# Kernel optimization log

Measured on AMD Instinct MI355X. Metric: run time of the kernel, lower is better.

## Reference

```python
import jax, jax.numpy as jnp
import numpy as np

EMB = 1024
HEADS = 16
HEAD_DIM = EMB // HEADS
BLOCK = 256
N_GLOBAL = 4
WINDOW = 128
ROPE_BASE = 10000.0


def rotate_half(x):
    # interleaved rotate: (-x2_0, x1_0, -x2_1, x1_1, ...), faithful to source
    x1 = x[..., ::2]
    x2 = x[..., 1::2]
    return jnp.stack((-x2, x1), axis=-1).reshape(x.shape)


def setup_inputs() -> dict:
    key = jax.random.key(0)
    k0, k1, k2 = jax.random.split(key, 3)
    B, S = 2, 2048
    x = jax.random.normal(k0, (B, S, EMB), dtype=jnp.float32)
    # Linear weights stored as [in, out]; y = x @ W (bias=False in source)
    w_qkv = jax.random.normal(k1, (EMB, 3 * EMB), dtype=jnp.float32) * (EMB ** -0.5)
    w_out = jax.random.normal(k2, (EMB, EMB), dtype=jnp.float32) * (EMB ** -0.5)
    return {"x": x, "w_qkv": w_qkv, "w_out": w_out}


def _forward(x, w_qkv, w_out):
    B, S, E = x.shape
    H, D = HEADS, HEAD_DIM
    qkv = (x @ w_qkv).reshape(B, S, 3, H, D).transpose(2, 0, 3, 1, 4)  # [3,B,H,S,D]
    q, k, v = qkv[0], qkv[1], qkv[2]

    # Rotary embedding (start_pos = 0, no cache)
    inv_freq = 1.0 / (ROPE_BASE ** (jnp.arange(0, D, 2, dtype=jnp.float32) / D))
    pos = jnp.arange(S, dtype=jnp.float32)
    freqs = jnp.outer(pos, inv_freq)                 # [S, D/2]
    emb = jnp.concatenate([freqs, freqs], axis=-1)   # [S, D]
    cos = jnp.cos(emb)[None, None]                   # [1,1,S,D]
    sin = jnp.sin(emb)[None, None]
    q = q * cos + rotate_half(q) * sin
    k = k * cos + rotate_half(k) * sin

    # Block-local + global-token + sliding-window mask, AND causal (vectorized)
    i = jnp.arange(S)[:, None]
    j = jnp.arange(S)[None, :]
    allowed = (i // BLOCK == j // BLOCK) | (i < N_GLOBAL) | (j < N_GLOBAL) \
              | (jnp.abs(i - j) <= WINDOW)
    allowed = allowed & (j <= i)
    # NOTE: source passes ~mask to F.scaled_dot_product_attention, where a
    # boolean attn_mask with True means "attend". We replicate that exactly.
    attend = ~allowed  # [S, S]

    scale = D ** -0.5
    scores = jnp.einsum("bhsd,bhtd->bhst", q, k) * scale      # [B,H,S,S]
    scores = jnp.where(attend[None, None], scores, jnp.float32(-1e30))
    attn = jax.nn.softmax(scores, axis=-1)
    out = jnp.einsum("bhst,bhtd->bhsd", attn, v)              # [B,H,S,D]
    out = out.transpose(0, 2, 1, 3).reshape(B, S, E)
    return out @ w_out


def reference(x, w_qkv, w_out):
    return _forward(x, w_qkv, w_out)
```

## Files before the change

kernel.cpp:

```cpp
#include <hip/hip_runtime.h>
#include <hip/hip_bf16.h>

#define EMBD   1024
#define NHEAD  16
#define HDIM   64
#define SEQ    2048
#define BATCH  2
#define MROWS  4096
#define NQKV   3072
#define VSTR   2064

using floatx4 = __attribute__((ext_vector_type(4))) float;
using short8  = __attribute__((ext_vector_type(8))) short;

static __device__ __forceinline__ float bf2f(unsigned short u) {
    unsigned int v = ((unsigned int)u) << 16;
    return __uint_as_float(v);
}
static __device__ __forceinline__ unsigned short f2bf(float f) {
    __hip_bfloat16 h = __float2bfloat16(f);
    return *reinterpret_cast<unsigned short*>(&h);
}

__global__ __launch_bounds__(256) void cast_x(
    const float* __restrict__ x, unsigned short* __restrict__ xh,
    unsigned short* __restrict__ xl)
{
    int idx = (blockIdx.x * 256 + threadIdx.x) * 4;
    float4 v = *(const float4*)(x + idx);
    ushort4 h, l;
    h.x = f2bf(v.x); l.x = f2bf(v.x - bf2f(h.x));
    h.y = f2bf(v.y); l.y = f2bf(v.y - bf2f(h.y));
    h.z = f2bf(v.z); l.z = f2bf(v.z - bf2f(h.z));
    h.w = f2bf(v.w); l.w = f2bf(v.w - bf2f(h.w));
    *(ushort4*)(xh + idx) = h;
    *(ushort4*)(xl + idx) = l;
}

__global__ __launch_bounds__(256) void cast_wT(
    const float* __restrict__ w, unsigned short* __restrict__ wT, int N)
{
    __shared__ unsigned short th[64][65];
    const int k0 = blockIdx.y * 64, n0 = blockIdx.x * 64;
    const int t = threadIdx.x;
    const int r = t >> 4, c = (t & 15) * 4;
    for (int rr = r; rr < 64; rr += 16) {
        float4 v = *(const float4*)(w + (size_t)(k0 + rr) * N + n0 + c);
        th[rr][c + 0] = f2bf(v.x);
        th[rr][c + 1] = f2bf(v.y);
        th[rr][c + 2] = f2bf(v.z);
        th[rr][c + 3] = f2bf(v.w);
    }
    __syncthreads();
    for (int rr = r; rr < 64; rr += 16) {
        ushort4 h;
        h.x = th[c + 0][rr]; h.y = th[c + 1][rr];
        h.z = th[c + 2][rr]; h.w = th[c + 3][rr];
        *(ushort4*)(wT + (size_t)(n0 + rr) * 1024 + k0 + c) = h;
    }
}

__global__ __launch_bounds__(256) void gemm_qkv_mfma(
    const unsigned short* __restrict__ xh, const unsigned short* __restrict__ xl,
    const unsigned short* __restrict__ wbT,
    unsigned short* __restrict__ qst, unsigned short* __restrict__ kst,
    unsigned short* __restrict__ vtT)
{
    const int t = threadIdx.x, wave = t >> 6, lane = t & 63;
    const int col = lane & 15, quad = lane >> 4;
    const int n0 = blockIdx.x * 128;
    const int m0 = blockIdx.y * 128;
    const int which = n0 >> 10;
    const int wm = (wave >> 1) * 64, wn = (wave & 1) * 64;

    floatx4 acc[4][4];
    #pragma unroll
    for (int i = 0; i < 4; ++i)
        #pragma unroll
        for (int j = 0; j < 4; ++j) acc[i][j] = (floatx4){0.f, 0.f, 0.f, 0.f};

    const unsigned short* pa_h = xh  + (size_t)(m0 + wm + col) * 1024 + quad * 8;
    const unsigned short* pa_l = xl  + (size_t)(m0 + wm + col) * 1024 + quad * 8;
    const unsigned short* pb   = wbT + (size_t)(n0 + wn + col) * 1024 + quad * 8;

    for (int k0 = 0; k0 < 1024; k0 += 32) {
        short8 bf[4], ah[4], al[4];
        #pragma unroll
        for (int f = 0; f < 4; ++f) bf[f] = *(const short8*)(pb   + f * 16 * 1024 + k0);
        #pragma unroll
        for (int f = 0; f < 4; ++f) ah[f] = *(const short8*)(pa_h + f * 16 * 1024 + k0);
        #pragma unroll
        for (int f = 0; f < 4; ++f) al[f] = *(const short8*)(pa_l + f * 16 * 1024 + k0);

        if (which < 2) {
            #pragma unroll
            for (int fm = 0; fm < 4; ++fm)
                #pragma unroll
                for (int fn = 0; fn < 4; ++fn) {
                    acc[fm][fn] = __builtin_amdgcn_mfma_f32_16x16x32_bf16(
                        bf[fn], ah[fm], acc[fm][fn], 0, 0, 0);
                    acc[fm][fn] = __builtin_amdgcn_mfma_f32_16x16x32_bf16(
                        bf[fn], al[fm], acc[fm][fn], 0, 0, 0);
                }
        } else {
            #pragma unroll
            for (int fm = 0; fm < 4; ++fm)
                #pragma unroll
                for (int fn = 0; fn < 4; ++fn) {
                    acc[fm][fn] = __builtin_amdgcn_mfma_f32_16x16x32_bf16(
                        ah[fm], bf[fn], acc[fm][fn], 0, 0, 0);
                    acc[fm][fn] = __builtin_amdgcn_mfma_f32_16x16x32_bf16(
                        al[fm], bf[fn], acc[fm][fn], 0, 0, 0);
                }
        }
    }

    const float RLOG = 9.210340371976184f / 32.0f;
    if (which < 2) {
        unsigned short* dst = (which == 0) ? qst : kst;
        const float scale = (which == 0) ? 0.125f : 1.0f;
        #pragma unroll
        for (int fm = 0; fm < 4; ++fm) {
            const int s_g = m0 + wm + fm * 16 + col;
            const int b = s_g >> 11, s = s_g & 2047;
            const float sf = (float)s;
            #pragma unroll
            for (int fn = 0; fn < 4; ++fn) {
                const int nl = (n0 & 1023) + wn + fn * 16 + quad * 4;
                const int h = nl >> 6;
                const int d0 = nl & 63;
                floatx4 c = acc[fm][fn];
                float o_[4];
                #pragma unroll
                for (int pp = 0; pp < 2; ++pp) {
                    int de = d0 + pp * 2;
                    float fe = __expf(-(float)(de & 31) * RLOG);
                    float fo = __expf(-(float)((de + 1) & 31) * RLOG);
                    float se, ce, so, co;
                    sincosf(sf * fe, &se, &ce);
                    sincosf(sf * fo, &so, &co);
                    float qe = c[pp * 2], qo = c[pp * 2 + 1];
                    o_[pp * 2]     = (qe * ce - qo * se) * scale;
                    o_[pp * 2 + 1] = (qo * co + qe * so) * scale;
                }
                ushort4 o4;
                o4.x = f2bf(o_[0]); o4.y = f2bf(o_[1]);
                o4.z = f2bf(o_[2]); o4.w = f2bf(o_[3]);
                *(ushort4*)(dst + ((size_t)(b * 16 + h) * 2048 + s) * 64 + d0) = o4;
            }
        }
    } else {
        #pragma unroll
        for (int fm = 0; fm < 4; ++fm) {
            const int m = m0 + wm + fm * 16 + quad * 4;
            const int b = m >> 11, s0 = m & 2047;
            #pragma unroll
            for (int fn = 0; fn < 4; ++fn) {
                const int nl = (n0 & 1023) + wn + fn * 16 + col;
                const int h = nl >> 6;
                const int d = nl & 63;
                floatx4 c = acc[fm][fn];
                ushort4 o4;
                o4.x = f2bf(c[0]); o4.y = f2bf(c[1]);
                o4.z = f2bf(c[2]); o4.w = f2bf(c[3]);
                *(ushort4*)(vtT + (size_t)(b * 16 + h) * 64 * VSTR
                                + (size_t)d * VSTR + s0) = o4;
            }
        }
    }
}

__global__ __launch_bounds__(256) void attn_mfma(
    const unsigned short* __restrict__ qst,
    const unsigned short* __restrict__ kst,
    const unsigned short* __restrict__ vtT,
    unsigned short* __restrict__ attn)
{
    __shared__ __attribute__((aligned(16))) unsigned short p_tile[2][4][16][40];
    __shared__ float4 redbuf[3][64][2][5];

    const int tid  = threadIdx.x;
    const int wave = tid >> 6;
    const int lane = tid & 63;
    const int col  = lane & 15;
    const int quad = lane >> 4;

    const int bh   = blockIdx.x >> 6;
    const int row0 = (blockIdx.x & 63) * 32;

    const size_t base  = (size_t)bh * SEQ * HDIM;
    const size_t vbase = (size_t)bh * HDIM * VSTR;

    short8 aq[2][2];
    #pragma unroll
    for (int tt = 0; tt < 2; ++tt) {
        const unsigned short* qp = qst + base
            + (size_t)(row0 + tt * 16 + col) * HDIM + quad * 8;
        aq[tt][0] = *(const short8*)(qp);
        aq[tt][1] = *(const short8*)(qp + 32);
    }

    int iR[2][4], ngR[2][4], j0R[2][4];
    #pragma unroll
    for (int tt = 0; tt < 2; ++tt)
        #pragma unroll
        for (int r = 0; r < 4; ++r) {
            int i = row0 + tt * 16 + quad * 4 + r;
            iR[tt][r] = i;
            ngR[tt][r] = (i + 1 < 4) ? (i + 1) : 4;
            int L = i - 128;
            int bs = (i >> 8) << 8;
            if (bs < L) L = bs;
            if (L < 0) L = 0;
            j0R[tt][r] = (L > 4) ? L : 4;
        }

    floatx4 o[2][4];
    float lsum[2][4];
    #pragma unroll
    for (int tt = 0; tt < 2; ++tt)
        #pragma unroll
        for (int r = 0; r < 4; ++r) {
            o[tt][r] = (floatx4){0.f, 0.f, 0.f, 0.f};
            lsum[tt][r] = 0.f;
        }

    const int kbeg = wave * (SEQ / 4);

    short8 kf[2][4];
    short8 vf[2][4];

#define LOADK(B, IT) do {                                                         \
        const int kc_ = kbeg + (IT) * 32;                                         \
        const unsigned short* kp_ = kst + base + (size_t)(kc_ + col) * HDIM       \
                                        + quad * 8;                               \
        kf[B][0] = *(const short8*)(kp_);                                         \
        kf[B][1] = *(const short8*)(kp_ + 32);                                    \
        kf[B][2] = *(const short8*)(kp_ + 16 * HDIM);                             \
        kf[B][3] = *(const short8*)(kp_ + 16 * HDIM + 32);                        \
    } while (0)
#define LOADV(B, IT) do {                                                         \
        const int kc_ = kbeg + (IT) * 32;                                         \
        const unsigned short* vp_ = vtT + vbase + (size_t)col * VSTR              \
                                        + kc_ + quad * 8;                         \
        vf[B][0] = *(const short8*)(vp_);                                         \
        vf[B][1] = *(const short8*)(vp_ + 16 * VSTR);                             \
        vf[B][2] = *(const short8*)(vp_ + 32 * VSTR);                             \
        vf[B][3] = *(const short8*)(vp_ + 48 * VSTR);                             \
    } while (0)

    LOADK(0, 0);
    LOADV(0, 0);
    #pragma unroll
    for (int it = 0; it < 16; ++it) {
        const int cur = it & 1;
        if (it < 15) { LOADK(cur ^ 1, it + 1); LOADV(cur ^ 1, it + 1); }
        __builtin_amdgcn_sched_barrier(0);

        const int kc0 = kbeg + it * 32;
        #pragma unroll
        for (int h16 = 0; h16 < 2; ++h16) {
            const int j = kc0 + h16 * 16 + col;
            #pragma unroll
            for (int tt = 0; tt < 2; ++tt) {
                floatx4 s = {0.f, 0.f, 0.f, 0.f};
                s = __builtin_amdgcn_mfma_f32_16x16x32_bf16(
                        aq[tt][0], kf[cur][h16 * 2 + 0], s, 0, 0, 0);
                s = __builtin_amdgcn_mfma_f32_16x16x32_bf16(
                        aq[tt][1], kf[cur][h16 * 2 + 1], s, 0, 0, 0);
                #pragma unroll
                for (int r = 0; r < 4; ++r) {
                    bool excl = (j < ngR[tt][r]) || (j >= j0R[tt][r] && j <= iR[tt][r]);
                    float p = excl ? 0.f : __expf(s[r]);
                    lsum[tt][r] += p;
                    p_tile[tt][wave][quad * 4 + r][h16 * 16 + col] = f2bf(p);
                }
            }
        }
        #pragma unroll
        for (int tt = 0; tt < 2; ++tt) {
            short8 ap = *(const short8*)&p_tile[tt][wave][col][quad * 8];
            o[tt][0] = __builtin_amdgcn_mfma_f32_16x16x32_bf16(ap, vf[cur][0], o[tt][0], 0, 0, 0);
            o[tt][1] = __builtin_amdgcn_mfma_f32_16x16x32_bf16(ap, vf[cur][1], o[tt][1], 0, 0, 0);
            o[tt][2] = __builtin_amdgcn_mfma_f32_16x16x32_bf16(ap, vf[cur][2], o[tt][2], 0, 0, 0);
            o[tt][3] = __builtin_amdgcn_mfma_f32_16x16x32_bf16(ap, vf[cur][3], o[tt][3], 0, 0, 0);
        }
    }
#undef LOADK
#undef LOADV

    #pragma unroll
    for (int tt = 0; tt < 2; ++tt)
        #pragma unroll
        for (int r = 0; r < 4; ++r) {
            float v = lsum[tt][r];
            v += __shfl_xor(v, 1);
            v += __shfl_xor(v, 2);
            v += __shfl_xor(v, 4);
            v += __shfl_xor(v, 8);
            lsum[tt][r] = v;
        }

    if (wave > 0) {
        #pragma unroll
        for (int tt = 0; tt < 2; ++tt) {
            redbuf[wave - 1][lane][tt][0] = make_float4(o[tt][0][0], o[tt][0][1], o[tt][0][2], o[tt][0][3]);
            redbuf[wave - 1][lane][tt][1] = make_float4(o[tt][1][0], o[tt][1][1], o[tt][1][2], o[tt][1][3]);
            redbuf[wave - 1][lane][tt][2] = make_float4(o[tt][2][0], o[tt][2][1], o[tt][2][2], o[tt][2][3]);
            redbuf[wave - 1][lane][tt][3] = make_float4(o[tt][3][0], o[tt][3][1], o[tt][3][2], o[tt][3][3]);
            redbuf[wave - 1][lane][tt][4] = make_float4(lsum[tt][0], lsum[tt][1], lsum[tt][2], lsum[tt][3]);
        }
    }
    __syncthreads();
    if (wave == 0) {
        #pragma unroll
        for (int w = 0; w < 3; ++w)
            #pragma unroll
            for (int tt = 0; tt < 2; ++tt) {
                float4 t0 = redbuf[w][lane][tt][0];
                float4 t1 = redbuf[w][lane][tt][1];
                float4 t2 = redbuf[w][lane][tt][2];
                float4 t3 = redbuf[w][lane][tt][3];
                float4 tl = redbuf[w][lane][tt][4];
                o[tt][0][0] += t0.x; o[tt][0][1] += t0.y; o[tt][0][2] += t0.z; o[tt][0][3] += t0.w;
                o[tt][1][0] += t1.x; o[tt][1][1] += t1.y; o[tt][1][2] += t1.z; o[tt][1][3] += t1.w;
                o[tt][2][0] += t2.x; o[tt][2][1] += t2.y; o[tt][2][2] += t2.z; o[tt][2][3] += t2.w;
                o[tt][3][0] += t3.x; o[tt][3][1] += t3.y; o[tt][3][2] += t3.z; o[tt][3][3] += t3.w;
                lsum[tt][0] += tl.x; lsum[tt][1] += tl.y; lsum[tt][2] += tl.z; lsum[tt][3] += tl.w;
            }
        const int b = bh >> 4, h = bh & 15;
        #pragma unroll
        for (int tt = 0; tt < 2; ++tt)
            #pragma unroll
            for (int r = 0; r < 4; ++r) {
                float inv = 1.0f / lsum[tt][r];
                unsigned short* orow = attn + ((size_t)(b * SEQ + iR[tt][r])) * EMBD
                                            + h * HDIM + col;
                orow[0]  = f2bf(o[tt][0][r] * inv);
                orow[16] = f2bf(o[tt][1][r] * inv);
                orow[32] = f2bf(o[tt][2][r] * inv);
                orow[48] = f2bf(o[tt][3][r] * inv);
            }
    }
}

__global__ __launch_bounds__(256) void gemm_out_mfma(
    const unsigned short* __restrict__ A,
    const unsigned short* __restrict__ woT,
    float* __restrict__ out)
{
    const int t = threadIdx.x, wave = t >> 6, lane = t & 63;
    const int col = lane & 15, quad = lane >> 4;
    const int n0 = blockIdx.x * 128;
    const int m0 = blockIdx.y * 128;
    const int wm = (wave >> 1) * 64, wn = (wave & 1) * 64;

    floatx4 acc[4][4];
    #pragma unroll
    for (int i = 0; i < 4; ++i)
        #pragma unroll
        for (int j = 0; j < 4; ++j) acc[i][j] = (floatx4){0.f, 0.f, 0.f, 0.f};

    const unsigned short* pa = A   + (size_t)(m0 + wm + col) * 1024 + quad * 8;
    const unsigned short* pb = woT + (size_t)(n0 + wn + col) * 1024 + quad * 8;

    for (int k0 = 0; k0 < 1024; k0 += 32) {
        short8 af[4], bf[4];
        #pragma unroll
        for (int f = 0; f < 4; ++f) bf[f] = *(const short8*)(pb + f * 16 * 1024 + k0);
        #pragma unroll
        for (int f = 0; f < 4; ++f) af[f] = *(const short8*)(pa + f * 16 * 1024 + k0);
        #pragma unroll
        for (int fm = 0; fm < 4; ++fm)
            #pragma unroll
            for (int fn = 0; fn < 4; ++fn)
                acc[fm][fn] = __builtin_amdgcn_mfma_f32_16x16x32_bf16(
                    af[fm], bf[fn], acc[fm][fn], 0, 0, 0);
    }

    #pragma unroll
    for (int fm = 0; fm < 4; ++fm) {
        const int m = m0 + wm + fm * 16 + quad * 4;
        #pragma unroll
        for (int fn = 0; fn < 4; ++fn) {
            const int n = n0 + wn + fn * 16 + col;
            floatx4 c = acc[fm][fn];
            out[(size_t)(m + 0) * 1024 + n] = c[0];
            out[(size_t)(m + 1) * 1024 + n] = c[1];
            out[(size_t)(m + 2) * 1024 + n] = c[2];
            out[(size_t)(m + 3) * 1024 + n] = c[3];
        }
    }
}

extern "C" void kernel_launch(void* const* d_in, const int* in_sizes, int n_in,
                              void* d_out, int out_size, void* d_ws, size_t ws_size,
                              hipStream_t stream) {
    const float* x     = (const float*)d_in[0];
    const float* w_qkv = (const float*)d_in[1];
    const float* w_out = (const float*)d_in[2];
    float* out = (float*)d_out;

    unsigned short* ws16 = (unsigned short*)d_ws;
    unsigned short* xh  = ws16;
    unsigned short* xl  = ws16 +  4194304;
    unsigned short* wbT = ws16 +  8388608;
    unsigned short* woT = ws16 + 11534336;
    unsigned short* qst = ws16 + 12582912;
    unsigned short* kst = ws16 + 16777216;
    unsigned short* vtT = ws16 + 20971520;
    unsigned short* aws = ws16 + 25198592;

    dim3 blk(256);
    cast_x<<<dim3(4096), blk, 0, stream>>>(x, xh, xl);
    cast_wT<<<dim3(48, 16), blk, 0, stream>>>(w_qkv, wbT, NQKV);
    cast_wT<<<dim3(16, 16), blk, 0, stream>>>(w_out, woT, EMBD);

    gemm_qkv_mfma<<<dim3(NQKV / 128, MROWS / 128), blk, 0, stream>>>(
        xh, xl, wbT, qst, kst, vtT);

    attn_mfma<<<dim3(32 * 64), blk, 0, stream>>>(qst, kst, vtT, aws);

    gemm_out_mfma<<<dim3(EMBD / 128, MROWS / 128), blk, 0, stream>>>(aws, woT, out);
}
```

Before: 367.0 us.

## Stage QKV GEMM operands through double-buffered LDS with direct global-to-LDS loads

The QKV projection GEMM no longer has each wave load its operand fragments straight from global memory. The block now cooperatively copies 128x32 tiles of x-high, x-low and the transposed weights into double-buffered shared memory using global_load_lds, prefetching the next K slice while MFMAs run on the current one. This lets waves in a block share operand loads instead of reading them redundantly, and hides global latency. In exchange it costs shared memory (48KB), which may limit occupancy, and adds a barrier per K step. LDS reads use an unpadded 64-byte row stride, which may cause bank conflicts.

After: 520.1 us. 41.7% more time.

```diff
diff --git a/kernel.cpp b/kernel.cpp
--- a/kernel.cpp
+++ b/kernel.cpp
@@ -20,6 +20,12 @@
 static __device__ __forceinline__ unsigned short f2bf(float f) {
     __hip_bfloat16 h = __float2bfloat16(f);
     return *reinterpret_cast<unsigned short*>(&h);
+}
+
+static __device__ __forceinline__ void gl_lds16(const void* g, void* l) {
+    __builtin_amdgcn_global_load_lds(
+        (const __attribute__((address_space(1))) unsigned int*)g,
+        (__attribute__((address_space(3))) unsigned int*)l, 16, 0, 0);
 }
 
 __global__ __launch_bounds__(256) void cast_x(
@@ -66,6 +72,10 @@
     unsigned short* __restrict__ qst, unsigned short* __restrict__ kst,
     unsigned short* __restrict__ vtT)
 {
+    __shared__ __attribute__((aligned(16))) unsigned short sAh[2][128][32];
+    __shared__ __attribute__((aligned(16))) unsigned short sAl[2][128][32];
+    __shared__ __attribute__((aligned(16))) unsigned short sB [2][128][32];
+
     const int t = threadIdx.x, wave = t >> 6, lane = t & 63;
     const int col = lane & 15, quad = lane >> 4;
     const int n0 = blockIdx.x * 128;
@@ -79,18 +89,35 @@
         #pragma unroll
         for (int j = 0; j < 4; ++j) acc[i][j] = (floatx4){0.f, 0.f, 0.f, 0.f};
 
-    const unsigned short* pa_h = xh  + (size_t)(m0 + wm + col) * 1024 + quad * 8;
-    const unsigned short* pa_l = xl  + (size_t)(m0 + wm + col) * 1024 + quad * 8;
-    const unsigned short* pb   = wbT + (size_t)(n0 + wn + col) * 1024 + quad * 8;
-
-    for (int k0 = 0; k0 < 1024; k0 += 32) {
+#define STAGE(B, K0) do {                                                         \
+        _Pragma("unroll")                                                         \
+        for (int c = 0; c < 2; ++c) {                                             \
+            const int idx = (wave * 2 + c) * 64 + lane;                           \
+            const int row = idx >> 2, seg = idx & 3;                              \
+            const int kk2 = (K0) + seg * 8;                                       \
+            unsigned short* lbase_a = &sAh[B][0][0] + (wave * 2 + c) * 512;       \
+            unsigned short* lbase_l = &sAl[B][0][0] + (wave * 2 + c) * 512;       \
+            unsigned short* lbase_b = &sB [B][0][0] + (wave * 2 + c) * 512;       \
+            gl_lds16(xh  + (size_t)(m0 + row) * 1024 + kk2, lbase_a);             \
+            gl_lds16(xl  + (size_t)(m0 + row) * 1024 + kk2, lbase_l);             \
+            gl_lds16(wbT + (size_t)(n0 + row) * 1024 + kk2, lbase_b);             \
+        }                                                                         \
+    } while (0)
+
+    STAGE(0, 0);
+    __syncthreads();
+    #pragma unroll
+    for (int kk = 0; kk < 32; ++kk) {
+        const int cur = kk & 1;
+        if (kk < 31) STAGE(cur ^ 1, (kk + 1) * 32);
+
         short8 bf[4], ah[4], al[4];
         #pragma unroll
-        for (int f = 0; f < 4; ++f) bf[f] = *(const short8*)(pb   + f * 16 * 1024 + k0);
-        #pragma unroll
-        for (int f = 0; f < 4; ++f) ah[f] = *(const short8*)(pa_h + f * 16 * 1024 + k0);
-        #pragma unroll
-        for (int f = 0; f < 4; ++f) al[f] = *(const short8*)(pa_l + f * 16 * 1024 + k0);
+        for (int f = 0; f < 4; ++f) {
+            bf[f] = *(const short8*)&sB [cur][wn + f * 16 + col][quad * 8];
+            ah[f] = *(const short8*)&sAh[cur][wm + f * 16 + col][quad * 8];
+            al[f] = *(const short8*)&sAl[cur][wm + f * 16 + col][quad * 8];
+        }
 
         if (which < 2) {
             #pragma unroll
@@ -113,7 +140,9 @@
                         al[fm], bf[fn], acc[fm][fn], 0, 0, 0);
                 }
         }
-    }
+        __syncthreads();
+    }
+#undef STAGE
 
     const float RLOG = 9.210340371976184f / 32.0f;
     if (which < 2) {
```

## Stage QKV GEMM operand tiles through LDS with register prefetch

Applied to the files above, without the earlier changes.

The QKV projection GEMM previously had each wave load its A (hi/lo) and B fragments straight from global memory, so every tile was fetched twice across the block's waves. Now the whole block cooperatively loads 128x32 tiles into shared memory, and the next k-step's global loads are prefetched into registers while MFMAs run on the current tile. This cuts redundant global traffic and hides latency, at the cost of two barriers per k-step and LDS reads that may bank-conflict on a 32-short row stride. The launch bound is also set to one block per SIMD minimum.

After: 472.9 us. +28.9%, slower.

```diff
diff --git a/kernel.cpp b/kernel.cpp
--- a/kernel.cpp
+++ b/kernel.cpp
@@ -60,12 +60,16 @@
     }
 }
 
-__global__ __launch_bounds__(256) void gemm_qkv_mfma(
+__global__ __launch_bounds__(256, 1) void gemm_qkv_mfma(
     const unsigned short* __restrict__ xh, const unsigned short* __restrict__ xl,
     const unsigned short* __restrict__ wbT,
     unsigned short* __restrict__ qst, unsigned short* __restrict__ kst,
     unsigned short* __restrict__ vtT)
 {
+    __shared__ __attribute__((aligned(16))) unsigned short sAh[128][32];
+    __shared__ __attribute__((aligned(16))) unsigned short sAl[128][32];
+    __shared__ __attribute__((aligned(16))) unsigned short sB [128][32];
+
     const int t = threadIdx.x, wave = t >> 6, lane = t & 63;
     const int col = lane & 15, quad = lane >> 4;
     const int n0 = blockIdx.x * 128;
@@ -79,18 +83,53 @@
         #pragma unroll
         for (int j = 0; j < 4; ++j) acc[i][j] = (floatx4){0.f, 0.f, 0.f, 0.f};
 
-    const unsigned short* pa_h = xh  + (size_t)(m0 + wm + col) * 1024 + quad * 8;
-    const unsigned short* pa_l = xl  + (size_t)(m0 + wm + col) * 1024 + quad * 8;
-    const unsigned short* pb   = wbT + (size_t)(n0 + wn + col) * 1024 + quad * 8;
-
+    const int srow = t >> 2;
+    const int scol = (t & 3) * 8;
+    const unsigned short* gAh0 = xh  + (size_t)(m0 + srow) * 1024 + scol;
+    const unsigned short* gAh1 = xh  + (size_t)(m0 + 64 + srow) * 1024 + scol;
+    const unsigned short* gAl0 = xl  + (size_t)(m0 + srow) * 1024 + scol;
+    const unsigned short* gAl1 = xl  + (size_t)(m0 + 64 + srow) * 1024 + scol;
+    const unsigned short* gB0  = wbT + (size_t)(n0 + srow) * 1024 + scol;
+    const unsigned short* gB1  = wbT + (size_t)(n0 + 64 + srow) * 1024 + scol;
+
+    short8 rh0, rh1, rl0, rl1, rb0, rb1;
+
+#define LOADSTAGE(K0) do {                                                        \
+        rh0 = *(const short8*)(gAh0 + (K0));                                      \
+        rh1 = *(const short8*)(gAh1 + (K0));                                      \
+        rl0 = *(const short8*)(gAl0 + (K0));                                      \
+        rl1 = *(const short8*)(gAl1 + (K0));                                      \
+        rb0 = *(const short8*)(gB0  + (K0));                                      \
+        rb1 = *(const short8*)(gB1  + (K0));                                      \
+    } while (0)
+
+#define WRITESTAGE() do {                                                         \
+        *(short8*)&sAh[srow][scol]      = rh0;                                    \
+        *(short8*)&sAh[64 + srow][scol] = rh1;                                    \
+        *(short8*)&sAl[srow][scol]      = rl0;                                    \
+        *(short8*)&sAl[64 + srow][scol] = rl1;                                    \
+        *(short8*)&sB [srow][scol]      = rb0;                                    \
+        *(short8*)&sB [64 + srow][scol] = rb1;                                    \
+    } while (0)
+
+    LOADSTAGE(0);
     for (int k0 = 0; k0 < 1024; k0 += 32) {
+        __syncthreads();
+        WRITESTAGE();
+        __syncthreads();
+        if (k0 + 32 < 1024) {
+            LOADSTAGE(k0 + 32);
+            asm volatile("" : "+v"(rh0), "+v"(rh1), "+v"(rl0),
+                              "+v"(rl1), "+v"(rb0), "+v"(rb1));
+        }
+
         short8 bf[4], ah[4], al[4];
         #pragma unroll
-        for (int f = 0; f < 4; ++f) bf[f] = *(const short8*)(pb   + f * 16 * 1024 + k0);
-        #pragma unroll
-        for (int f = 0; f < 4; ++f) ah[f] = *(const short8*)(pa_h + f * 16 * 1024 + k0);
-        #pragma unroll
-        for (int f = 0; f < 4; ++f) al[f] = *(const short8*)(pa_l + f * 16 * 1024 + k0);
+        for (int f = 0; f < 4; ++f) {
+            bf[f] = *(const short8*)&sB [wn + f * 16 + col][quad * 8];
+            ah[f] = *(const short8*)&sAh[wm + f * 16 + col][quad * 8];
+            al[f] = *(const short8*)&sAl[wm + f * 16 + col][quad * 8];
+        }
 
         if (which < 2) {
             #pragma unroll
@@ -114,6 +153,8 @@
                 }
         }
     }
+#undef LOADSTAGE
+#undef WRITESTAGE
 
     const float RLOG = 9.210340371976184f / 32.0f;
     if (which < 2) {
```
